# Optimization experiments

Hardware: AMD Instinct MI355X
Metric: run time of the kernel (lower is better)

The kernel has to match this reference:

```python
import jax, jax.numpy as jnp
import numpy as np

B, T, D_IN = 32, 32, 128
N_SLOTS, M_LEN = 512, 64
NUM_SHIFT, NUM_READ, NUM_WRITE = 3, 4, 1
CTRL_DIM = 256
READ_HEAD_LEN = 3 + M_LEN + NUM_SHIFT            # k, beta, g, s, gamma
WRITE_HEAD_LEN = READ_HEAD_LEN + 2 * M_LEN       # + erase, add vectors
INSTR_DIM = NUM_READ * READ_HEAD_LEN + NUM_WRITE * WRITE_HEAD_LEN


def setup_inputs() -> dict:
    key = jax.random.key(0)
    ks = jax.random.split(key, 4)
    def glorot(k, shape):
        lim = np.sqrt(6.0 / (shape[0] + shape[1])).astype(np.float32)
        return jax.random.uniform(k, shape, jnp.float32, -lim, lim)
    return {
        "x": jax.random.normal(ks[0], (B, T, D_IN), jnp.float32),
        "Wc": glorot(ks[1], (D_IN + NUM_READ * M_LEN, CTRL_DIM)),
        "bc": jnp.zeros((CTRL_DIM,), jnp.float32),
        "heads_kernel": glorot(ks[2], (CTRL_DIM, INSTR_DIM)),
        "heads_bias": jnp.zeros((INSTR_DIM,), jnp.float32),
    }


def _parse_heads(h):
    # h: (B, H, 3 + M + S) -> k, beta, g, s, gamma per _get_weight_vector
    k = h[..., :M_LEN]
    b = jnp.exp(h[..., M_LEN])
    g = jax.nn.sigmoid(h[..., M_LEN + 1])
    s = jax.nn.softmax(h[..., M_LEN + 2:M_LEN + 2 + NUM_SHIFT], axis=-1)
    t = jax.nn.softplus(h[..., M_LEN + 2 + NUM_SHIFT]) + 1.0
    return k, b, g, s, t


def _address(Mem, w_prev, k, b, g, s, t):
    # Mem:(B,N,M) k:(B,H,M) w_prev:(B,H,N) b,g,t:(B,H) s:(B,H,S)
    eps = 1e-8
    Mn = jnp.linalg.norm(Mem, axis=-1)                       # (B,N)
    kn = jnp.linalg.norm(k, axis=-1)                         # (B,H)
    sim = jnp.einsum('bhm,bnm->bhn', k, Mem) / (kn[..., None] * Mn[:, None, :] + eps)
    wc = jax.nn.softmax(b[..., None] * sim, axis=-1)         # content
    wg = g[..., None] * wc + (1.0 - g[..., None]) * w_prev   # gate
    half = NUM_SHIFT // 2                                    # circular shift conv
    wsh = sum(s[..., i:i + 1] * jnp.roll(wg, i - half, axis=-1) for i in range(NUM_SHIFT))
    wt = wsh ** t[..., None]                                 # sharpen
    return wt / (jnp.sum(wt, axis=-1, keepdims=True) + eps)


def _ntm_forward(x, Wc, bc, heads_kernel, heads_bias):
    def step(carry, x_t):
        r, rw, ww, Mem = carry
        # dense controller on [x_t, old read vectors]
        ctrl_in = jnp.concatenate([x_t, r.reshape(B, -1)], axis=-1)
        h = jnp.tanh(ctrl_in @ Wc + bc)                      # controller_out == instr
        instr = h @ heads_kernel + heads_bias                # (B, INSTR_DIM)
        rh = instr[:, :NUM_READ * READ_HEAD_LEN].reshape(B, NUM_READ, READ_HEAD_LEN)
        wh = instr[:, NUM_READ * READ_HEAD_LEN:].reshape(B, NUM_WRITE, WRITE_HEAD_LEN)
        rw_n = _address(Mem, rw, *_parse_heads(rh))
        ww_n = _address(Mem, ww, *_parse_heads(wh[..., :READ_HEAD_LEN]))
        e = wh[..., READ_HEAD_LEN:READ_HEAD_LEN + M_LEN]     # raw erase (no sigmoid, as in source)
        a = wh[..., READ_HEAD_LEN + M_LEN:]                  # raw add
        # erase all heads, then add all heads (source loops erase first)
        Mem = Mem * jnp.prod(1.0 - ww_n[..., :, None] * e[..., None, :], axis=1)
        Mem = Mem + jnp.einsum('bwn,bwm->bnm', ww_n, a)
        r_n = jnp.einsum('bnm,brn->brm', Mem, rw_n)          # read
        return (r_n, rw_n, ww_n, Mem), h

    init = (jnp.zeros((B, NUM_READ, M_LEN), jnp.float32),
            jnp.zeros((B, NUM_READ, N_SLOTS), jnp.float32),
            jnp.zeros((B, NUM_WRITE, N_SLOTS), jnp.float32),
            jnp.zeros((B, N_SLOTS, M_LEN), jnp.float32))
    _, outs = jax.lax.scan(step, init, jnp.swapaxes(x, 0, 1))  # time-major
    return outs[-1]  # return_sequences=False -> last controller output (B, CTRL_DIM)


def reference(x, Wc, bc, heads_kernel, heads_bias):
    return _ntm_forward(x, Wc, bc, heads_kernel, heads_bias)
```

## Files before the change

kernel.cpp:

```cpp
#include <hip/hip_runtime.h>
#include <math.h>

#define BB 32
#define TT 32
#define D_INX 128
#define NSLOT 512
#define MLEN 64
#define NREAD 4
#define NHEAD 5
#define CDIM 256
#define IDIM 478
#define RHL 70
#define NT 512

#define HKB_OFF 196608

struct SMem {
    float mem[NSLOT * MLEN];
    float wprev[NHEAD * NSLOT];
    float mn[NSLOT];
    float ctrl[384];
    float h[CDIM];
    float instr[480];
    float k[NHEAD * MLEN];
    float e[MLEN];
    float a[MLEN];
    float u[2560];
};

__device__ __forceinline__ unsigned short f2bf(float f) {
    unsigned u = __float_as_uint(f);
    return (unsigned short)((u + 0x7fffu + ((u >> 16) & 1u)) >> 16);
}

__global__ void pack_kernel(const float* __restrict__ Wc, const float* __restrict__ Hk,
                            unsigned short* __restrict__ wctb, unsigned short* __restrict__ hkb)
{
    int idx = blockIdx.x * 256 + threadIdx.x;
    if (idx < 384 * 256) {
        int i = idx >> 8, col = idx & 255;
        wctb[((i >> 3) * 256 + col) * 8 + (i & 7)] = f2bf(Wc[idx]);
    }
    if (idx < 256 * 478) {
        int i = idx / 478, col = idx - i * 478;
        hkb[((i >> 3) * 478 + col) * 8 + (i & 7)] = f2bf(Hk[idx]);
    }
}

#define BF8_DOT(wv, c0, c1, c2, c3, acc) do {                                   \
    unsigned _u0 = __float_as_uint((wv).x), _u1 = __float_as_uint((wv).y);      \
    unsigned _u2 = __float_as_uint((wv).z), _u3 = __float_as_uint((wv).w);      \
    acc += __uint_as_float(_u0 << 16) * (c0).x + __uint_as_float(_u0 & 0xffff0000u) * (c0).y; \
    acc += __uint_as_float(_u1 << 16) * (c1).x + __uint_as_float(_u1 & 0xffff0000u) * (c1).y; \
    acc += __uint_as_float(_u2 << 16) * (c2).x + __uint_as_float(_u2 & 0xffff0000u) * (c2).y; \
    acc += __uint_as_float(_u3 << 16) * (c3).x + __uint_as_float(_u3 & 0xffff0000u) * (c3).y; \
} while (0)

__global__ __launch_bounds__(NT, 2)
void ntm_kernel(const float* __restrict__ x,
                const float* __restrict__ bc,
                const float* __restrict__ hb,
                const unsigned short* __restrict__ wctb,
                const unsigned short* __restrict__ hkb,
                float* __restrict__ out)
{
    extern __shared__ float smem_f[];
    SMem* sc = (SMem*)smem_f;

    const int b    = blockIdx.x;
    const int tid  = threadIdx.x;
    const int lane = tid & 63;
    const int wave = tid >> 6;

    const float bcv = (tid < CDIM) ? bc[tid] : 0.f;
    const float hbv = (tid < IDIM) ? hb[tid] : 0.f;

    {
        float4 z4 = make_float4(0.f, 0.f, 0.f, 0.f);
        float4* m4 = (float4*)sc->mem;
        for (int i = tid; i < NSLOT * MLEN / 4; i += NT) m4[i] = z4;
        for (int i = tid; i < NHEAD * NSLOT; i += NT) sc->wprev[i] = 0.f;
        sc->mn[tid] = 0.f;
        if (tid < 384) sc->ctrl[tid] = (tid < D_INX) ? x[(size_t)b * TT * D_INX + tid] : 0.f;
    }
    __syncthreads();

    for (int t = 0; t < TT; ++t) {
        {
            int col = tid & 255, kb = tid >> 8;
            const float4* wq = (const float4*)wctb + kb * 24 * 256 + col;
            const float2* c2 = (const float2*)sc->ctrl + kb * 96;
            float acc = 0.f;
#pragma unroll
            for (int cc = 0; cc < 24; ++cc) {
                float4 wv = wq[cc * 256];
                float2 x0 = c2[cc * 4], x1 = c2[cc * 4 + 1], x2 = c2[cc * 4 + 2], x3 = c2[cc * 4 + 3];
                BF8_DOT(wv, x0, x1, x2, x3, acc);
            }
            sc->u[kb * 256 + col] = acc;
        }
        __syncthreads();

        if (tid < CDIM) {
            float hv = tanhf(bcv + sc->u[tid] + sc->u[256 + tid]);
            sc->h[tid] = hv;
            if (t == TT - 1) out[(size_t)b * CDIM + tid] = hv;
        } else if (tid < 384 && t + 1 < TT) {
            sc->ctrl[tid - 256] = x[((size_t)b * TT + t + 1) * D_INX + (tid - 256)];
        }
        if (t == TT - 1) break;
        __syncthreads();

        if (tid < IDIM) {
            const float4* wq = (const float4*)hkb + tid;
            const float2* h2 = (const float2*)sc->h;
            float acc = hbv;
#pragma unroll
            for (int c = 0; c < 32; ++c) {
                float4 wv = wq[c * 478];
                float2 x0 = h2[c * 4], x1 = h2[c * 4 + 1], x2 = h2[c * 4 + 2], x3 = h2[c * 4 + 3];
                BF8_DOT(wv, x0, x1, x2, x3, acc);
            }
            sc->instr[tid] = acc;
            if (tid < 350) {
                int hh = (tid * 937) >> 16;
                int m = tid - hh * RHL;
                if (m < MLEN) sc->k[hh * MLEN + m] = acc;
            } else if (tid < 414) {
                sc->e[tid - 350] = acc;
            } else {
                sc->a[tid - 414] = acc;
            }
        }
        __syncthreads();

        {
            int n = tid, nx = n & 15;
            const float4* m4 = (const float4*)sc->mem + n * 16;
            const float4* k4 = (const float4*)sc->k;
            float d0 = 0.f, d1 = 0.f, d2 = 0.f, d3 = 0.f, d4 = 0.f;
#pragma unroll
            for (int j = 0; j < 16; ++j) {
                float4 mv = m4[j ^ nx];
                float4 k0 = k4[j], k1 = k4[16 + j], k2 = k4[32 + j], k3 = k4[48 + j], kw = k4[64 + j];
                d0 += mv.x * k0.x + mv.y * k0.y + mv.z * k0.z + mv.w * k0.w;
                d1 += mv.x * k1.x + mv.y * k1.y + mv.z * k1.z + mv.w * k1.w;
                d2 += mv.x * k2.x + mv.y * k2.y + mv.z * k2.z + mv.w * k2.w;
                d3 += mv.x * k3.x + mv.y * k3.y + mv.z * k3.z + mv.w * k3.w;
                d4 += mv.x * kw.x + mv.y * kw.y + mv.z * kw.z + mv.w * kw.w;
            }
            sc->u[n] = d0; sc->u[512 + n] = d1; sc->u[1024 + n] = d2;
            sc->u[1536 + n] = d3; sc->u[2048 + n] = d4;
        }
        __syncthreads();

        if (wave < NHEAD) {
            const int h = wave;
            const float* ins = sc->instr + h * RHL;
            float kv = ins[lane];
            float sq = kv * kv;
#pragma unroll
            for (int off = 32; off; off >>= 1) sq += __shfl_xor(sq, off);
            float kn = sqrtf(sq);
            float beta = __expf(ins[64]);
            float g = 1.f / (1.f + __expf(-ins[65]));
            float v0 = ins[66], v1 = ins[67], v2 = ins[68];
            float mx3 = fmaxf(v0, fmaxf(v1, v2));
            float e0 = __expf(v0 - mx3), e1 = __expf(v1 - mx3), e2 = __expf(v2 - mx3);
            float inv3 = 1.f / (e0 + e1 + e2);
            float s0 = e0 * inv3, s1 = e1 * inv3, s2 = e2 * inv3;
            float tv = ins[69];
            float tp = fmaxf(tv, 0.f) + log1pf(__expf(-fabsf(tv))) + 1.f;

            float uu[8];
#pragma unroll
            for (int j = 0; j < 8; ++j) {
                int slot = j * 64 + lane;
                float d = sc->u[h * NSLOT + slot];
                uu[j] = beta * d / (kn * sc->mn[slot] + 1e-8f);
            }
            float m = uu[0];
#pragma unroll
            for (int j = 1; j < 8; ++j) m = fmaxf(m, uu[j]);
#pragma unroll
            for (int off = 32; off; off >>= 1) m = fmaxf(m, __shfl_xor(m, off));
            float ev[8]; float Z = 0.f;
#pragma unroll
            for (int j = 0; j < 8; ++j) { ev[j] = __expf(uu[j] - m); Z += ev[j]; }
#pragma unroll
            for (int off = 32; off; off >>= 1) Z += __shfl_xor(Z, off);
            float invZ = 1.f / Z;
            float wg[8];
#pragma unroll
            for (int j = 0; j < 8; ++j) {
                int slot = j * 64 + lane;
                wg[j] = g * ev[j] * invZ + (1.f - g) * sc->wprev[h * NSLOT + slot];
            }
            int lm = (lane + 63) & 63, lp = (lane + 1) & 63;
            float rm[8], rp[8], b63[8], b0[8];
#pragma unroll
            for (int j = 0; j < 8; ++j) {
                rm[j]  = __shfl(wg[j], lm);
                rp[j]  = __shfl(wg[j], lp);
                b63[j] = __shfl(wg[j], 63);
                b0[j]  = __shfl(wg[j], 0);
            }
            if (lane == 0) {
#pragma unroll
                for (int j = 0; j < 8; ++j) rm[j] = b63[(j + 7) & 7];
            }
            if (lane == 63) {
#pragma unroll
                for (int j = 0; j < 8; ++j) rp[j] = b0[(j + 1) & 7];
            }
            float wt[8]; float S = 0.f;
#pragma unroll
            for (int j = 0; j < 8; ++j) {
                float wsh = s0 * rp[j] + s1 * wg[j] + s2 * rm[j];
                wt[j] = __builtin_amdgcn_exp2f(tp * __builtin_amdgcn_logf(wsh));
                S += wt[j];
            }
#pragma unroll
            for (int off = 32; off; off >>= 1) S += __shfl_xor(S, off);
            float invS = 1.f / (S + 1e-8f);
#pragma unroll
            for (int j = 0; j < 8; ++j)
                sc->wprev[h * NSLOT + j * 64 + lane] = wt[j] * invS;
        }
        __syncthreads();

        {
            int n = tid, nx = n & 15;
            float4* m4 = (float4*)sc->mem + n * 16;
            const float4* e4 = (const float4*)sc->e;
            const float4* a4 = (const float4*)sc->a;
            float wv = sc->wprev[4 * NSLOT + n];
            float nsq = 0.f;
#pragma unroll
            for (int j = 0; j < 16; ++j) {
                float4 mv = m4[j ^ nx];
                float4 ev = e4[j], av = a4[j];
                mv.x = mv.x * (1.f - wv * ev.x) + wv * av.x;
                mv.y = mv.y * (1.f - wv * ev.y) + wv * av.y;
                mv.z = mv.z * (1.f - wv * ev.z) + wv * av.z;
                mv.w = mv.w * (1.f - wv * ev.w) + wv * av.w;
                nsq += mv.x * mv.x + mv.y * mv.y + mv.z * mv.z + mv.w * mv.w;
                m4[j ^ nx] = mv;
            }
            sc->mn[n] = sqrtf(nsq);
        }
        __syncthreads();

        {
            int rg = lane >> 4, j = lane & 15;
            int base = wave * 64;
            float4 ac[4];
#pragma unroll
            for (int hh = 0; hh < 4; ++hh) ac[hh] = make_float4(0.f, 0.f, 0.f, 0.f);
#pragma unroll
            for (int i = 0; i < 16; ++i) {
                int n = base + 4 * i + rg;
                float4 mv = ((const float4*)sc->mem)[n * 16 + (j ^ (n & 15))];
                float w0 = sc->wprev[n], w1 = sc->wprev[512 + n];
                float w2 = sc->wprev[1024 + n], w3 = sc->wprev[1536 + n];
                ac[0].x += w0 * mv.x; ac[0].y += w0 * mv.y; ac[0].z += w0 * mv.z; ac[0].w += w0 * mv.w;
                ac[1].x += w1 * mv.x; ac[1].y += w1 * mv.y; ac[1].z += w1 * mv.z; ac[1].w += w1 * mv.w;
                ac[2].x += w2 * mv.x; ac[2].y += w2 * mv.y; ac[2].z += w2 * mv.z; ac[2].w += w2 * mv.w;
                ac[3].x += w3 * mv.x; ac[3].y += w3 * mv.y; ac[3].z += w3 * mv.z; ac[3].w += w3 * mv.w;
            }
            float* af = (float*)ac;
#pragma unroll
            for (int q = 0; q < 16; ++q) {
                af[q] += __shfl_xor(af[q], 16);
                af[q] += __shfl_xor(af[q], 32);
            }
            if (rg == 0) {
                float4* rp = (float4*)(sc->u + wave * 256);
                rp[0 * 16 + j] = ac[0];
                rp[1 * 16 + j] = ac[1];
                rp[2 * 16 + j] = ac[2];
                rp[3 * 16 + j] = ac[3];
            }
        }
        __syncthreads();

        if (tid < 256) {
            float s = 0.f;
#pragma unroll
            for (int w = 0; w < 8; ++w) s += sc->u[w * 256 + tid];
            sc->ctrl[128 + tid] = s;
        }
        __syncthreads();
    }
}

extern "C" void kernel_launch(void* const* d_in, const int* in_sizes, int n_in,
                              void* d_out, int out_size, void* d_ws, size_t ws_size,
                              hipStream_t stream) {
    const float* x  = (const float*)d_in[0];
    const float* Wc = (const float*)d_in[1];
    const float* bc = (const float*)d_in[2];
    const float* Hk = (const float*)d_in[3];
    const float* hb = (const float*)d_in[4];
    float* out = (float*)d_out;

    unsigned short* wctb = (unsigned short*)d_ws;
    unsigned short* hkb  = (unsigned short*)((char*)d_ws + HKB_OFF);

    static_assert(sizeof(SMem) <= 163840, "LDS overflow");
    (void)hipFuncSetAttribute((const void*)ntm_kernel,
                              hipFuncAttributeMaxDynamicSharedMemorySize,
                              (int)sizeof(SMem));

    hipLaunchKernelGGL(pack_kernel, dim3(478), dim3(256), 0, stream, Wc, Hk, wctb, hkb);
    hipLaunchKernelGGL(ntm_kernel, dim3(BB), dim3(NT), sizeof(SMem), stream,
                       x, bc, hb, wctb, hkb, out);
}
```

Baseline: 905.4 us.

## Fuse controller matvec with tanh, double-buffer input, interleave read weights

The controller matvec now runs in 256 threads, each accumulating the full 384-length dot product. This drops the two-way K split, the partial-sum buffer and one block barrier per timestep. The next x_t is loaded into a double-buffered ctrl region with float4 loads. Read-head weights are stored interleaved per slot, so the read phase fetches all four weights with one float4 load. tanh and softplus now use hardware exp2/log intrinsics. The tradeoff is that only half of the threads do the controller matvec, giving each one a longer serial chain, and the fast intrinsics are slightly less precise.

```diff
diff --git a/kernel.cpp b/kernel.cpp
--- a/kernel.cpp
+++ b/kernel.cpp
@@ -17,9 +17,10 @@
 
 struct SMem {
     float mem[NSLOT * MLEN];
-    float wprev[NHEAD * NSLOT];
+    float wread4[NSLOT * 4];
+    float wwrite[NSLOT];
     float mn[NSLOT];
-    float ctrl[384];
+    float ctrl[512];
     float h[CDIM];
     float instr[480];
     float k[NHEAD * MLEN];
@@ -47,14 +48,16 @@
     }
 }
 
-#define BF8_DOT(wv, c0, c1, c2, c3, acc) do {                                   \
-    unsigned _u0 = __float_as_uint((wv).x), _u1 = __float_as_uint((wv).y);      \
-    unsigned _u2 = __float_as_uint((wv).z), _u3 = __float_as_uint((wv).w);      \
-    acc += __uint_as_float(_u0 << 16) * (c0).x + __uint_as_float(_u0 & 0xffff0000u) * (c0).y; \
-    acc += __uint_as_float(_u1 << 16) * (c1).x + __uint_as_float(_u1 & 0xffff0000u) * (c1).y; \
-    acc += __uint_as_float(_u2 << 16) * (c2).x + __uint_as_float(_u2 & 0xffff0000u) * (c2).y; \
-    acc += __uint_as_float(_u3 << 16) * (c3).x + __uint_as_float(_u3 & 0xffff0000u) * (c3).y; \
+#define BFU_DOT(wv, cA, cB, acc) do {                                           \
+    unsigned _u0 = (wv).x, _u1 = (wv).y, _u2 = (wv).z, _u3 = (wv).w;            \
+    acc += __uint_as_float(_u0 << 16) * (cA).x + __uint_as_float(_u0 & 0xffff0000u) * (cA).y; \
+    acc += __uint_as_float(_u1 << 16) * (cA).z + __uint_as_float(_u1 & 0xffff0000u) * (cA).w; \
+    acc += __uint_as_float(_u2 << 16) * (cB).x + __uint_as_float(_u2 & 0xffff0000u) * (cB).y; \
+    acc += __uint_as_float(_u3 << 16) * (cB).z + __uint_as_float(_u3 & 0xffff0000u) * (cB).w; \
 } while (0)
+
+#define L2E 1.4426950408889634f
+#define LN2 0.6931471805599453f
 
 __global__ __launch_bounds__(NT, 2)
 void ntm_kernel(const float* __restrict__ x,
@@ -79,47 +82,54 @@
         float4 z4 = make_float4(0.f, 0.f, 0.f, 0.f);
         float4* m4 = (float4*)sc->mem;
         for (int i = tid; i < NSLOT * MLEN / 4; i += NT) m4[i] = z4;
-        for (int i = tid; i < NHEAD * NSLOT; i += NT) sc->wprev[i] = 0.f;
+        ((float4*)sc->wread4)[tid] = z4;
+        sc->wwrite[tid] = 0.f;
         sc->mn[tid] = 0.f;
-        if (tid < 384) sc->ctrl[tid] = (tid < D_INX) ? x[(size_t)b * TT * D_INX + tid] : 0.f;
+        sc->ctrl[tid] = (tid < D_INX) ? x[(size_t)b * TT * D_INX + tid] : 0.f;
     }
     __syncthreads();
 
     for (int t = 0; t < TT; ++t) {
-        {
-            int col = tid & 255, kb = tid >> 8;
-            const float4* wq = (const float4*)wctb + kb * 24 * 256 + col;
-            const float2* c2 = (const float2*)sc->ctrl + kb * 96;
-            float acc = 0.f;
-#pragma unroll
-            for (int cc = 0; cc < 24; ++cc) {
-                float4 wv = wq[cc * 256];
-                float2 x0 = c2[cc * 4], x1 = c2[cc * 4 + 1], x2 = c2[cc * 4 + 2], x3 = c2[cc * 4 + 3];
-                BF8_DOT(wv, x0, x1, x2, x3, acc);
-            }
-            sc->u[kb * 256 + col] = acc;
-        }
-        __syncthreads();
-
         if (tid < CDIM) {
-            float hv = tanhf(bcv + sc->u[tid] + sc->u[256 + tid]);
+            const uint4* wq = (const uint4*)wctb + tid;
+            const float4* xa = (const float4*)(sc->ctrl + ((t & 1) << 7));
+            const float4* ra = (const float4*)(sc->ctrl + 256);
+            float acc = bcv;
+#pragma unroll
+            for (int cc = 0; cc < 16; ++cc) {
+                uint4 wv = wq[cc * 256];
+                float4 cA = xa[2 * cc], cB = xa[2 * cc + 1];
+                BFU_DOT(wv, cA, cB, acc);
+            }
+#pragma unroll
+            for (int cc = 16; cc < 48; ++cc) {
+                uint4 wv = wq[cc * 256];
+                float4 cA = ra[2 * (cc - 16)], cB = ra[2 * (cc - 16) + 1];
+                BFU_DOT(wv, cA, cB, acc);
+            }
+            float av = fabsf(acc);
+            float ex = __builtin_amdgcn_exp2f(av * (2.f * L2E));
+            float r1 = 1.f - 2.f / (ex + 1.f);
+            float hv = (acc < 0.f) ? -r1 : r1;
             sc->h[tid] = hv;
             if (t == TT - 1) out[(size_t)b * CDIM + tid] = hv;
-        } else if (tid < 384 && t + 1 < TT) {
-            sc->ctrl[tid - 256] = x[((size_t)b * TT + t + 1) * D_INX + (tid - 256)];
+        } else if (tid < 288 && t + 1 < TT) {
+            int i = tid - 256;
+            ((float4*)(sc->ctrl + (((t + 1) & 1) << 7)))[i] =
+                ((const float4*)(x + ((size_t)b * TT + t + 1) * D_INX))[i];
         }
         if (t == TT - 1) break;
         __syncthreads();
 
         if (tid < IDIM) {
-            const float4* wq = (const float4*)hkb + tid;
-            const float2* h2 = (const float2*)sc->h;
+            const uint4* wq = (const uint4*)hkb + tid;
+            const float4* h4 = (const float4*)sc->h;
             float acc = hbv;
 #pragma unroll
             for (int c = 0; c < 32; ++c) {
-                float4 wv = wq[c * 478];
-                float2 x0 = h2[c * 4], x1 = h2[c * 4 + 1], x2 = h2[c * 4 + 2], x3 = h2[c * 4 + 3];
-                BF8_DOT(wv, x0, x1, x2, x3, acc);
+                uint4 wv = wq[c * IDIM];
+                float4 cA = h4[2 * c], cB = h4[2 * c + 1];
+                BFU_DOT(wv, cA, cB, acc);
             }
             sc->instr[tid] = acc;
             if (tid < 350) {
@@ -170,7 +180,9 @@
             float inv3 = 1.f / (e0 + e1 + e2);
             float s0 = e0 * inv3, s1 = e1 * inv3, s2 = e2 * inv3;
             float tv = ins[69];
-            float tp = fmaxf(tv, 0.f) + log1pf(__expf(-fabsf(tv))) + 1.f;
+            float tp = fmaxf(tv, 0.f)
+                     + LN2 * __builtin_amdgcn_logf(1.f + __builtin_amdgcn_exp2f(-fabsf(tv) * L2E))
+                     + 1.f;
 
             float uu[8];
 #pragma unroll
@@ -193,8 +205,9 @@
             float wg[8];
 #pragma unroll
             for (int j = 0; j < 8; ++j) {
-                int slot = j * 64 + lane;
-                wg[j] = g * ev[j] * invZ + (1.f - g) * sc->wprev[h * NSLOT + slot];
+                int n = j * 64 + lane;
+                float wp = (h < 4) ? sc->wread4[n * 4 + h] : sc->wwrite[n];
+                wg[j] = g * ev[j] * invZ + (1.f - g) * wp;
             }
             int lm = (lane + 63) & 63, lp = (lane + 1) & 63;
             float rm[8], rp[8], b63[8], b0[8];
@@ -223,9 +236,15 @@
 #pragma unroll
             for (int off = 32; off; off >>= 1) S += __shfl_xor(S, off);
             float invS = 1.f / (S + 1e-8f);
-#pragma unroll
-            for (int j = 0; j < 8; ++j)
-                sc->wprev[h * NSLOT + j * 64 + lane] = wt[j] * invS;
+            if (h < 4) {
+#pragma unroll
+                for (int j = 0; j < 8; ++j)
+                    sc->wread4[(j * 64 + lane) * 4 + h] = wt[j] * invS;
+            } else {
+#pragma unroll
+                for (int j = 0; j < 8; ++j)
+                    sc->wwrite[j * 64 + lane] = wt[j] * invS;
+            }
         }
         __syncthreads();
 
@@ -234,7 +253,7 @@
             float4* m4 = (float4*)sc->mem + n * 16;
             const float4* e4 = (const float4*)sc->e;
             const float4* a4 = (const float4*)sc->a;
-            float wv = sc->wprev[4 * NSLOT + n];
+            float wv = sc->wwrite[n];
             float nsq = 0.f;
 #pragma unroll
             for (int j = 0; j < 16; ++j) {
@@ -261,12 +280,11 @@
             for (int i = 0; i < 16; ++i) {
                 int n = base + 4 * i + rg;
                 float4 mv = ((const float4*)sc->mem)[n * 16 + (j ^ (n & 15))];
-                float w0 = sc->wprev[n], w1 = sc->wprev[512 + n];
-                float w2 = sc->wprev[1024 + n], w3 = sc->wprev[1536 + n];
-                ac[0].x += w0 * mv.x; ac[0].y += w0 * mv.y; ac[0].z += w0 * mv.z; ac[0].w += w0 * mv.w;
-                ac[1].x += w1 * mv.x; ac[1].y += w1 * mv.y; ac[1].z += w1 * mv.z; ac[1].w += w1 * mv.w;
-                ac[2].x += w2 * mv.x; ac[2].y += w2 * mv.y; ac[2].z += w2 * mv.z; ac[2].w += w2 * mv.w;
-                ac[3].x += w3 * mv.x; ac[3].y += w3 * mv.y; ac[3].z += w3 * mv.z; ac[3].w += w3 * mv.w;
+                float4 wv = ((const float4*)sc->wread4)[n];
+                ac[0].x += wv.x * mv.x; ac[0].y += wv.x * mv.y; ac[0].z += wv.x * mv.z; ac[0].w += wv.x * mv.w;
+                ac[1].x += wv.y * mv.x; ac[1].y += wv.y * mv.y; ac[1].z += wv.y * mv.z; ac[1].w += wv.y * mv.w;
+                ac[2].x += wv.z * mv.x; ac[2].y += wv.z * mv.y; ac[2].z += wv.z * mv.z; ac[2].w += wv.z * mv.w;
+                ac[3].x += wv.w * mv.x; ac[3].y += wv.w * mv.y; ac[3].z += wv.w * mv.z; ac[3].w += wv.w * mv.w;
             }
             float* af = (float*)ac;
 #pragma unroll
@@ -288,7 +306,7 @@
             float s = 0.f;
 #pragma unroll
             for (int w = 0; w < 8; ++w) s += sc->u[w * 256 + tid];
-            sc->ctrl[128 + tid] = s;
+            sc->ctrl[256 + tid] = s;
         }
         __syncthreads();
     }
```

Result: slower. 965.7 us (+6.7%).
